# Performance work log

Hardware: AMD Instinct MI355X
Metric: run time of the kernel (lower is better)

## Reference

```python
import jax, jax.numpy as jnp
import numpy as np

N, E, F = 50000, 1_600_000, 128
EPS = 1e-5
DATASET_NUM = 1.0


def _glorot(k, shape):
    lim = jnp.sqrt(6.0 / (shape[0] + shape[1]))
    return jax.random.uniform(k, shape, jnp.float32, -lim, lim)


def setup_inputs() -> dict:
    key = jax.random.key(0)
    ks = jax.random.split(key, 24)
    inp = {
        "x": jax.random.normal(ks[0], (N, F), jnp.float32),
        "noise": jax.random.normal(ks[1], (N, F), jnp.float32),
        "edge_index": jax.random.randint(ks[2], (2, E), 0, N, jnp.int64),
        # ChebConv K=2 weights: W0 (T_0 = x term), W1 (T_1 = L_hat x term)
        "W1_0": _glorot(ks[3], (F, 64)),  "W1_1": _glorot(ks[4], (F, 64)),  "b1": jnp.zeros((64,), jnp.float32),
        "g1": jnp.ones((64,), jnp.float32), "be1": jnp.zeros((64,), jnp.float32),
        "W2_0": _glorot(ks[5], (64, 16)), "W2_1": _glorot(ks[6], (64, 16)), "b2": jnp.zeros((16,), jnp.float32),
        "W3_0": _glorot(ks[7], (16, 64)), "W3_1": _glorot(ks[8], (16, 64)), "b3": jnp.zeros((64,), jnp.float32),
        "g3": jnp.ones((64,), jnp.float32), "be3": jnp.zeros((64,), jnp.float32),
        "W4_0": _glorot(ks[9], (64, F)),  "W4_1": _glorot(ks[10], (64, F)), "b4": jnp.zeros((F,), jnp.float32),
    }
    return inp


def reference(x, noise, edge_index, W1_0, W1_1, b1, g1, be1,
              W2_0, W2_1, b2, W3_0, W3_1, b3, g3, be3, W4_0, W4_1, b4):
    src, dst = edge_index[0], edge_index[1]
    n = x.shape[0]

    # train-mode noise injection: x + dataset_num * randn * x.mean()
    x = x + DATASET_NUM * noise * jnp.mean(x)

    # symmetric normalization; with lambda_max=2 the scaled Laplacian is -A_norm
    deg = jax.ops.segment_sum(jnp.ones_like(src, dtype=x.dtype), dst, num_segments=n)
    dinv = jnp.where(deg > 0, jax.lax.rsqrt(jnp.maximum(deg, 1.0)), 0.0)
    w_e = dinv[src] * dinv[dst]  # [E]

    def cheb(h, W0, W1, b):
        # T_0 = h ; T_1 = L_hat h = -A_norm h  (K=2 ChebConv)
        tx1 = -jax.ops.segment_sum(w_e[:, None] * h[src], dst, num_segments=n)
        return h @ W0 + tx1 @ W1 + b

    def bn(h, g, be):
        mu = jnp.mean(h, axis=0)
        var = jnp.mean((h - mu) ** 2, axis=0)
        return g * (h - mu) * jax.lax.rsqrt(var + EPS) + be

    h1 = jax.nn.relu(bn(cheb(x, W1_0, W1_1, b1), g1, be1))
    h2 = cheb(h1, W2_0, W2_1, b2)
    h3 = jax.nn.relu(bn(cheb(h2, W3_0, W3_1, b3), g3, be3))
    return cheb(h3, W4_0, W4_1, b4)
```

## Files before the change

kernel.cpp:

```cpp
#include <hip/hip_runtime.h>

#define NNODES 50000
#define NEDGES 1600000
#define FEAT   128
#define EPSV   1e-5f
#define NBUCK  ((NNODES + 511) / 512)

typedef _Float16 h8 __attribute__((ext_vector_type(8)));
typedef _Float16 h4 __attribute__((ext_vector_type(4)));

__device__ __forceinline__ float4 f4fma(float s, float4 w, float4 a) {
  a.x = fmaf(s, w.x, a.x); a.y = fmaf(s, w.y, a.y);
  a.z = fmaf(s, w.z, a.z); a.w = fmaf(s, w.w, a.w);
  return a;
}

__global__ __launch_bounds__(256) void sum_kernel(const float* __restrict__ x,
                                                  float* __restrict__ out, int n4) {
  const float4* x4 = (const float4*)x;
  float s = 0.f;
  for (int i = blockIdx.x * blockDim.x + threadIdx.x; i < n4; i += gridDim.x * blockDim.x) {
    float4 v = x4[i];
    s += v.x + v.y + v.z + v.w;
  }
  for (int off = 32; off > 0; off >>= 1) s += __shfl_down(s, off);
  __shared__ float ls[4];
  int wid = threadIdx.x >> 6;
  if ((threadIdx.x & 63) == 0) ls[wid] = s;
  __syncthreads();
  if (threadIdx.x == 0) atomicAdd(out, ls[0] + ls[1] + ls[2] + ls[3]);
}

__global__ __launch_bounds__(256) void degree_kernel(const int* __restrict__ ei,
                                                     int* __restrict__ degi, int ne) {
  int e = blockIdx.x * blockDim.x + threadIdx.x;
  if (e < ne) atomicAdd(&degi[ei[NEDGES + e]], 1);
}

__global__ __launch_bounds__(256) void dinv_kernel(const int* __restrict__ degi,
                                                   float* __restrict__ dinv, int n) {
  int i = blockIdx.x * blockDim.x + threadIdx.x;
  if (i < n) dinv[i] = (degi[i] > 0) ? rsqrtf((float)degi[i]) : 0.f;
}

__global__ __launch_bounds__(1024) void scan1_kernel(const int* __restrict__ cnt,
                                                     int* __restrict__ exc,
                                                     int* __restrict__ bsum, int n) {
  __shared__ int s[1024];
  int tid = threadIdx.x;
  int i = blockIdx.x * 1024 + tid;
  int v = (i < n) ? cnt[i] : 0;
  int val = v;
  s[tid] = v;
  __syncthreads();
  for (int off = 1; off < 1024; off <<= 1) {
    int t = (tid >= off) ? s[tid - off] : 0;
    __syncthreads();
    val += t;
    s[tid] = val;
    __syncthreads();
  }
  if (i < n) exc[i] = val - v;
  if (tid == 1023) bsum[blockIdx.x] = val;
}

__global__ __launch_bounds__(256) void scan2_kernel(int* __restrict__ bsum, int nb) {
  __shared__ int s[256];
  int tid = threadIdx.x;
  int v = (tid < nb) ? bsum[tid] : 0;
  int val = v;
  s[tid] = v;
  __syncthreads();
  for (int off = 1; off < 256; off <<= 1) {
    int t = (tid >= off) ? s[tid - off] : 0;
    __syncthreads();
    val += t;
    s[tid] = val;
    __syncthreads();
  }
  if (tid < nb) bsum[tid] = val - v;
}

__global__ __launch_bounds__(256) void scan3_kernel(int* __restrict__ row_ptr,
                                                    const int* __restrict__ bsum,
                                                    int* __restrict__ cursor,
                                                    int* __restrict__ gcur, int n) {
  int i = blockIdx.x * blockDim.x + threadIdx.x;
  if (i < n) {
    int v = row_ptr[i] + bsum[i >> 10];
    row_ptr[i] = v;
    cursor[i] = v;
    if ((i & 511) == 0) gcur[i >> 9] = v;
  } else if (i == n) {
    row_ptr[n] = NEDGES;
  }
}

__global__ __launch_bounds__(256) void binA_kernel(const int* __restrict__ ei,
                                                   int* __restrict__ gcur,
                                                   unsigned int* __restrict__ gstage,
                                                   int ne) {
  __shared__ int hist[NBUCK];
  __shared__ int prefix[NBUCK + 1];
  __shared__ int offs[NBUCK];
  __shared__ int gbase[NBUCK];
  __shared__ unsigned int stag[4096];
  const int tid = threadIdx.x;
  const int c0 = blockIdx.x * 4096;
  for (int b = tid; b < NBUCK; b += 256) hist[b] = 0;
  __syncthreads();
  for (int i = tid; i < 4096; i += 256) {
    int e = c0 + i;
    if (e < ne) atomicAdd(&hist[ei[NEDGES + e] >> 9], 1);
  }
  __syncthreads();
  if (tid == 0) {
    int s = 0;
    for (int b = 0; b < NBUCK; ++b) { prefix[b] = s; s += hist[b]; }
    prefix[NBUCK] = s;
  }
  __syncthreads();
  if (tid < NBUCK) {
    offs[tid] = prefix[tid];
    gbase[tid] = atomicAdd(&gcur[tid], hist[tid]);
  }
  __syncthreads();
  for (int i = tid; i < 4096; i += 256) {
    int e = c0 + i;
    if (e < ne) {
      int s = ei[e];
      int d = ei[NEDGES + e];
      int b = d >> 9;
      int p = atomicAdd(&offs[b], 1);
      stag[p] = (unsigned int)s | ((unsigned int)(d & 511) << 16);
    }
  }
  __syncthreads();
  const int total = prefix[NBUCK];
  for (int j = tid; j < total; j += 256) {
    int lo = 0, hi = NBUCK;
    while (hi - lo > 1) {
      int mid = (lo + hi) >> 1;
      if (prefix[mid] <= j) lo = mid; else hi = mid;
    }
    gstage[gbase[lo] + (j - prefix[lo])] = stag[j];
  }
}

__global__ __launch_bounds__(1024) void binB_kernel(const unsigned int* __restrict__ gstage,
                                                    const int* __restrict__ row_ptr,
                                                    const float* __restrict__ dinv,
                                                    int* __restrict__ cursor,
                                                    int2* __restrict__ ep, int n) {
  const int b = blockIdx.x;
  const int node0 = b << 9;
  const int node1 = min(n, node0 + 512);
  const int start = row_ptr[node0];
  const int end = row_ptr[node1];
  for (int i = start + threadIdx.x; i < end; i += 1024) {
    unsigned int v = gstage[i];
    int s = (int)(v & 0xFFFFu);
    int d = node0 + (int)(v >> 16);
    float w = dinv[s] * dinv[d];
    int pos = atomicAdd(&cursor[d], 1);
    ep[pos] = make_int2(s, __float_as_int(w));
  }
}

template <int F, bool ADD, bool STATS, bool BNIN, bool OUTH>
__global__ __launch_bounds__(256) void spmm_kernel(
    const int* __restrict__ row_ptr, const int2* __restrict__ ep,
    const _Float16* __restrict__ gsrc, const float* __restrict__ addL,
    const float* __restrict__ bias,
    const float* __restrict__ stats_in, const float* __restrict__ gin,
    const float* __restrict__ bein, float* __restrict__ stats_out,
    void* __restrict__ outv, int n) {
  constexpr int LPE = F / 8;
  constexpr int EPC = 64 / LPE;
  constexpr int LG  = (LPE == 2) ? 1 : 3;
  __shared__ float sst[STATS ? 2 * F : 1];
  const int tid = threadIdx.x;
  if (STATS) {
    if (tid < 2 * F) sst[tid] = 0.f;
    __syncthreads();
  }
  const int lane = tid & 63;
  const int wv = tid >> 6;
  const int sub = lane & (LPE - 1);
  const int g = lane >> LG;
  const int f0 = sub * 8;
  float scl[8], sht[8];
  if (BNIN) {
    const float inv_n = 1.0f / (float)n;
#pragma unroll
    for (int j = 0; j < 8; ++j) {
      int f = f0 + j;
      float mu = stats_in[f] * inv_n;
      float var = stats_in[F + f] * inv_n - mu * mu;
      float s = gin[f] * rsqrtf(var + EPSV);
      scl[j] = s;
      sht[j] = bein[f] - mu * s;
    }
  }
  for (int node = blockIdx.x * 4 + wv; node < n; node += gridDim.x * 4) {
    float acc[8] = {};
    const int beg = row_ptr[node], end = row_ptr[node + 1];
    int e = beg + g;
    while (e < end) {
      int2 s0 = ep[e];
      bool p1 = (e + EPC) < end;
      int2 s1 = ep[p1 ? e + EPC : e];
      float w0 = __int_as_float(s0.y);
      float w1 = p1 ? __int_as_float(s1.y) : 0.f;
      h8 r0 = *(const h8*)(gsrc + (size_t)s0.x * F + f0);
      h8 r1 = *(const h8*)(gsrc + (size_t)s1.x * F + f0);
#pragma unroll
      for (int j = 0; j < 8; ++j) {
        float v0 = (float)r0[j], v1 = (float)r1[j];
        if (BNIN) {
          v0 = fmaxf(fmaf(v0, scl[j], sht[j]), 0.f);
          v1 = fmaxf(fmaf(v1, scl[j], sht[j]), 0.f);
        }
        acc[j] = fmaf(w0, v0, acc[j]);
        acc[j] = fmaf(w1, v1, acc[j]);
      }
      e += 2 * EPC;
    }
#pragma unroll
    for (int m = LPE; m < 64; m <<= 1) {
#pragma unroll
      for (int j = 0; j < 8; ++j) acc[j] += __shfl_xor(acc[j], m);
    }
    if (lane < LPE) {
      float o[8];
      if (ADD) {
        float4 a0 = *(const float4*)&addL[(size_t)node * F + f0];
        float4 a1 = *(const float4*)&addL[(size_t)node * F + f0 + 4];
        float4 b0 = *(const float4*)&bias[f0];
        float4 b1 = *(const float4*)&bias[f0 + 4];
        o[0] = a0.x + b0.x - acc[0]; o[1] = a0.y + b0.y - acc[1];
        o[2] = a0.z + b0.z - acc[2]; o[3] = a0.w + b0.w - acc[3];
        o[4] = a1.x + b1.x - acc[4]; o[5] = a1.y + b1.y - acc[5];
        o[6] = a1.z + b1.z - acc[6]; o[7] = a1.w + b1.w - acc[7];
      } else {
#pragma unroll
        for (int j = 0; j < 8; ++j) o[j] = -acc[j];
      }
      if (OUTH) {
        h8 ho;
#pragma unroll
        for (int j = 0; j < 8; ++j) ho[j] = (_Float16)o[j];
        *(h8*)((_Float16*)outv + (size_t)node * F + f0) = ho;
      } else {
        float* op = (float*)outv + (size_t)node * F + f0;
        *(float4*)op = make_float4(o[0], o[1], o[2], o[3]);
        *(float4*)(op + 4) = make_float4(o[4], o[5], o[6], o[7]);
      }
      if (STATS) {
#pragma unroll
        for (int j = 0; j < 8; ++j) {
          atomicAdd(&sst[f0 + j], o[j]);
          atomicAdd(&sst[F + f0 + j], o[j] * o[j]);
        }
      }
    }
  }
  if (STATS) {
    __syncthreads();
    if (tid < 2 * F) atomicAdd(&stats_out[tid], sst[tid]);
  }
}

template <int K, int NB, bool ROWCAT, bool BIAS, bool BNIN, bool STATS, bool NOISE,
          bool A1H, int OMODE>
__global__ __launch_bounds__(256) void gemm_kernel(
    const void* __restrict__ A1, const float* __restrict__ A2,
    const float* __restrict__ W0, const float* __restrict__ W1,
    const float* __restrict__ bias, int col0, int wnt, int ostride, int ocol0,
    const float* __restrict__ noise, const float* __restrict__ sumv,
    const float* __restrict__ stats_in, const float* __restrict__ gin,
    const float* __restrict__ bein, float* __restrict__ stats_out,
    void* __restrict__ outv, void* __restrict__ out2, int n) {
  constexpr int TC  = NB / 4;
  constexpr int RG  = 256 / TC;
  constexpr int RPT = 4;
  constexpr int RPB = RG * RPT;
  constexpr int AP  = K + 4;
  constexpr int KB  = ROWCAT ? K / 2 : K;
  __shared__ float wl[K * NB];
  __shared__ float al[RPB * AP];
  __shared__ float sarr[BNIN ? KB : 1];
  __shared__ float tarr[BNIN ? KB : 1];
  __shared__ float sst[STATS ? 2 * NB : 1];
  const int tid = threadIdx.x;
  if (STATS && tid < 2 * NB) sst[tid] = 0.f;
  if (BNIN) {
    const float inv_n = 1.0f / (float)n;
    for (int f = tid; f < KB; f += 256) {
      float mu = stats_in[f] * inv_n;
      float var = stats_in[KB + f] * inv_n - mu * mu;
      float s = gin[f] * rsqrtf(var + EPSV);
      sarr[f] = s;
      tarr[f] = bein[f] - mu * s;
    }
  }
  float mean = 0.f;
  if (NOISE) mean = sumv[0] * (1.0f / (float)(NNODES * FEAT));

  for (int i = tid; i < K * NB; i += 256) {
    int k = i / NB, j = i - k * NB;
    int jg = col0 + j;
    float v;
    if (ROWCAT) v = (k < K / 2) ? W0[k * wnt + jg] : W1[(k - K / 2) * wnt + jg];
    else        v = (jg < wnt / 2) ? W0[k * (wnt / 2) + jg] : W1[k * (wnt / 2) + (jg - wnt / 2)];
    wl[i] = v;
  }
  __syncthreads();

  const int row0 = blockIdx.x * RPB;
  for (int i = tid; i < RPB * K; i += 256) {
    int r = i / K, k = i - r * K;
    int gr = row0 + r;
    float v = 0.f;
    if (gr < n) {
      if (ROWCAT) {
        if (k < K / 2) {
          v = A1H ? (float)((const _Float16*)A1)[(size_t)gr * (K / 2) + k]
                  : ((const float*)A1)[(size_t)gr * (K / 2) + k];
          if (BNIN) v = fmaxf(fmaf(v, sarr[k], tarr[k]), 0.f);
        } else {
          v = A2[(size_t)gr * (K / 2) + (k - K / 2)];
        }
      } else {
        v = A1H ? (float)((const _Float16*)A1)[(size_t)gr * K + k]
                : ((const float*)A1)[(size_t)gr * K + k];
        if (BNIN) v = fmaxf(fmaf(v, sarr[k], tarr[k]), 0.f);
        if (NOISE) v = fmaf(noise[(size_t)gr * K + k], mean, v);
      }
    }
    al[r * AP + k] = v;
  }
  __syncthreads();

  const int jt = (tid % TC) * 4;
  const int rbase = (tid / TC) * RPT;
  float4 acc[RPT];
#pragma unroll
  for (int rr = 0; rr < RPT; ++rr) acc[rr] = make_float4(0.f, 0.f, 0.f, 0.f);
  const float4* wl4 = (const float4*)wl;
  const int jt4 = jt >> 2;
#pragma unroll 4
  for (int k0 = 0; k0 < K; k0 += 4) {
    float4 w0 = wl4[(k0 + 0) * TC + jt4];
    float4 w1 = wl4[(k0 + 1) * TC + jt4];
    float4 w2 = wl4[(k0 + 2) * TC + jt4];
    float4 w3 = wl4[(k0 + 3) * TC + jt4];
#pragma unroll
    for (int rr = 0; rr < RPT; ++rr) {
      float4 a = *(const float4*)&al[(rbase + rr) * AP + k0];
      acc[rr] = f4fma(a.x, w0, acc[rr]);
      acc[rr] = f4fma(a.y, w1, acc[rr]);
      acc[rr] = f4fma(a.z, w2, acc[rr]);
      acc[rr] = f4fma(a.w, w3, acc[rr]);
    }
  }
  float4 b4 = make_float4(0.f, 0.f, 0.f, 0.f);
  if (BIAS) b4 = *(const float4*)&bias[col0 + jt];
  float sl[4] = {}, ql[4] = {};
#pragma unroll
  for (int rr = 0; rr < RPT; ++rr) {
    int gr = row0 + rbase + rr;
    if (gr < n) {
      float4 o;
      o.x = acc[rr].x + b4.x; o.y = acc[rr].y + b4.y;
      o.z = acc[rr].z + b4.z; o.w = acc[rr].w + b4.w;
      if (OMODE == 0) {
        *(float4*)((float*)outv + (size_t)gr * ostride + ocol0 + jt) = o;
      } else if (OMODE == 1) {
        h4 ho; ho[0] = (_Float16)o.x; ho[1] = (_Float16)o.y;
        ho[2] = (_Float16)o.z; ho[3] = (_Float16)o.w;
        *(h4*)((_Float16*)outv + (size_t)gr * ostride + ocol0 + jt) = ho;
      } else {
        if (jt < 16) {
          *(float4*)((float*)outv + (size_t)gr * 16 + jt) = o;
        } else {
          h4 ho; ho[0] = (_Float16)o.x; ho[1] = (_Float16)o.y;
          ho[2] = (_Float16)o.z; ho[3] = (_Float16)o.w;
          *(h4*)((_Float16*)out2 + (size_t)gr * 16 + (jt - 16)) = ho;
        }
      }
      if (STATS) {
        sl[0] += o.x; ql[0] += o.x * o.x; sl[1] += o.y; ql[1] += o.y * o.y;
        sl[2] += o.z; ql[2] += o.z * o.z; sl[3] += o.w; ql[3] += o.w * o.w;
      }
    }
  }
  if (STATS) {
#pragma unroll
    for (int j = 0; j < 4; ++j) {
      atomicAdd(&sst[jt + j], sl[j]);
      atomicAdd(&sst[NB + jt + j], ql[j]);
    }
    __syncthreads();
    if (tid < 2 * NB) atomicAdd(&stats_out[tid], sst[tid]);
  }
}

extern "C" void kernel_launch(void* const* d_in, const int* in_sizes, int n_in,
                              void* d_out, int out_size, void* d_ws, size_t ws_size,
                              hipStream_t stream) {
  const float* x     = (const float*)d_in[0];
  const float* noise = (const float*)d_in[1];
  const int*   ei    = (const int*)d_in[2];
  const float* W1_0 = (const float*)d_in[3];
  const float* W1_1 = (const float*)d_in[4];
  const float* b1   = (const float*)d_in[5];
  const float* g1   = (const float*)d_in[6];
  const float* be1  = (const float*)d_in[7];
  const float* W2_0 = (const float*)d_in[8];
  const float* W2_1 = (const float*)d_in[9];
  const float* b2   = (const float*)d_in[10];
  const float* W3_0 = (const float*)d_in[11];
  const float* W3_1 = (const float*)d_in[12];
  const float* b3   = (const float*)d_in[13];
  const float* g3   = (const float*)d_in[14];
  const float* be3  = (const float*)d_in[15];
  const float* W4_0 = (const float*)d_in[16];
  const float* W4_1 = (const float*)d_in[17];
  const float* b4   = (const float*)d_in[18];
  float* out = (float*)d_out;

  char* p = (char*)d_ws;
  size_t off = 0;
  auto alloc = [&](size_t b) -> void* {
    void* r = p + off;
    off += (b + 255) & ~(size_t)255;
    return r;
  };
  float* s_sum  = (float*)alloc(4);
  float* stats0 = (float*)alloc(2 * 64 * 4);
  float* stats1 = (float*)alloc(2 * 64 * 4);
  int*   degi   = (int*)alloc(sizeof(int) * NNODES);
  size_t zero_bytes = off;
  float*     dinv    = (float*)alloc(sizeof(float) * NNODES);
  int*       row_ptr = (int*)alloc(sizeof(int) * (NNODES + 1));
  int*       bsum    = (int*)alloc(256 * sizeof(int));
  int*       cursor  = (int*)alloc(sizeof(int) * NNODES);
  int*       gcur    = (int*)alloc(sizeof(int) * NBUCK);
  int2*      ep      = (int2*)alloc(8ULL * NEDGES);
  float*     zzL     = (float*)alloc(4ULL * NNODES * 64);
  _Float16*  zzRh    = (_Float16*)alloc(2ULL * NNODES * 64);
  float*     h1      = (float*)alloc(4ULL * NNODES * 64);
  _Float16*  zz2Rh   = (_Float16*)alloc(2ULL * NNODES * 16);
  _Float16*  h2      = (_Float16*)alloc(2ULL * NNODES * 16);
  _Float16*  h3h     = (_Float16*)alloc(2ULL * NNODES * 64);
  float*     agg4    = zzL;

  unsigned int* gstage = (unsigned int*)out;
  float* zz2L = out;
  float* agg3 = out + (size_t)NNODES * 16;

  hipMemsetAsync(d_ws, 0, zero_bytes, stream);

  int n4 = NNODES * FEAT / 4;
  sum_kernel<<<2048, 256, 0, stream>>>(x, s_sum, n4);
  degree_kernel<<<(NEDGES + 255) / 256, 256, 0, stream>>>(ei, degi, NEDGES);
  dinv_kernel<<<(NNODES + 255) / 256, 256, 0, stream>>>(degi, dinv, NNODES);
  scan1_kernel<<<(NNODES + 1023) / 1024, 1024, 0, stream>>>(degi, row_ptr, bsum, NNODES);
  scan2_kernel<<<1, 256, 0, stream>>>(bsum, (NNODES + 1023) / 1024);
  scan3_kernel<<<(NNODES + 256) / 256, 256, 0, stream>>>(row_ptr, bsum, cursor, gcur, NNODES);
  binA_kernel<<<(NEDGES + 4095) / 4096, 256, 0, stream>>>(ei, gcur, gstage, NEDGES);
  binB_kernel<<<NBUCK, 1024, 0, stream>>>(gstage, row_ptr, dinv, cursor, ep, NNODES);

  gemm_kernel<128, 64, false, false, false, false, true, false, 0>
      <<<(NNODES + 63) / 64, 256, 0, stream>>>(
      x, nullptr, W1_0, W1_1, nullptr, 0, 128, 64, 0,
      noise, s_sum, nullptr, nullptr, nullptr, nullptr, zzL, nullptr, NNODES);
  gemm_kernel<128, 64, false, false, false, false, true, false, 1>
      <<<(NNODES + 63) / 64, 256, 0, stream>>>(
      x, nullptr, W1_0, W1_1, nullptr, 64, 128, 64, 0,
      noise, s_sum, nullptr, nullptr, nullptr, nullptr, zzRh, nullptr, NNODES);
  spmm_kernel<64, true, true, false, false><<<2048, 256, 0, stream>>>(
      row_ptr, ep, zzRh, zzL, b1, nullptr, nullptr, nullptr, stats0, h1, NNODES);

  gemm_kernel<64, 32, false, false, true, false, false, false, 2>
      <<<(NNODES + 127) / 128, 256, 0, stream>>>(
      h1, nullptr, W2_0, W2_1, nullptr, 0, 32, 16, 0,
      nullptr, nullptr, stats0, g1, be1, nullptr, zz2L, zz2Rh, NNODES);
  spmm_kernel<16, true, false, false, true><<<2048, 256, 0, stream>>>(
      row_ptr, ep, zz2Rh, zz2L, b2, nullptr, nullptr, nullptr, nullptr, h2, NNODES);

  spmm_kernel<16, false, false, false, false><<<2048, 256, 0, stream>>>(
      row_ptr, ep, h2, nullptr, nullptr, nullptr, nullptr, nullptr, nullptr, agg3, NNODES);
  gemm_kernel<32, 64, true, true, false, true, false, true, 1>
      <<<(NNODES + 63) / 64, 256, 0, stream>>>(
      h2, agg3, W3_0, W3_1, b3, 0, 64, 64, 0,
      nullptr, nullptr, nullptr, nullptr, nullptr, stats1, h3h, nullptr, NNODES);

  spmm_kernel<64, false, false, true, false><<<2048, 256, 0, stream>>>(
      row_ptr, ep, h3h, nullptr, nullptr, stats1, g3, be3, nullptr, agg4, NNODES);
  gemm_kernel<128, 64, true, true, true, false, false, true, 0>
      <<<(NNODES + 63) / 64, 256, 0, stream>>>(
      h3h, agg4, W4_0, W4_1, b4, 0, 128, 128, 0,
      nullptr, nullptr, stats1, g3, be3, nullptr, out, nullptr, NNODES);
  gemm_kernel<128, 64, true, true, true, false, false, true, 0>
      <<<(NNODES + 63) / 64, 256, 0, stream>>>(
      h3h, agg4, W4_0, W4_1, b4, 64, 128, 128, 64,
      nullptr, nullptr, stats1, g3, be3, nullptr, out, nullptr, NNODES);
}
```

Baseline: 688.5 us.

## Factor edge weights into source/destination scaling and compress edge list to 16-bit

Drops the per-edge normalisation weight by factoring dinv[src]*dinv[dst] into a pre-scale of source rows (in the GEMM epilogue or a dual-output SpMM) and a post-scale by dinv[dst]. The edge list shrinks from 8-byte (index, weight) pairs to 16-bit source indices, and several intermediates (zzL, h1, agg3, agg4) move from fp32 to fp16. This cuts gather and streaming bandwidth in the SpMMs and GEMMs, at the cost of more fp16 rounding and reliance on node indices fitting in 16 bits. The BN-input SpMM still gathers dinv per edge, because the ReLU prevents pre-scaling there.

```diff
diff --git a/kernel.cpp b/kernel.cpp
--- a/kernel.cpp
+++ b/kernel.cpp
@@ -149,9 +149,8 @@
 
 __global__ __launch_bounds__(1024) void binB_kernel(const unsigned int* __restrict__ gstage,
                                                     const int* __restrict__ row_ptr,
-                                                    const float* __restrict__ dinv,
                                                     int* __restrict__ cursor,
-                                                    int2* __restrict__ ep, int n) {
+                                                    unsigned short* __restrict__ ep, int n) {
   const int b = blockIdx.x;
   const int node0 = b << 9;
   const int node1 = min(n, node0 + 512);
@@ -161,20 +160,19 @@
     unsigned int v = gstage[i];
     int s = (int)(v & 0xFFFFu);
     int d = node0 + (int)(v >> 16);
-    float w = dinv[s] * dinv[d];
     int pos = atomicAdd(&cursor[d], 1);
-    ep[pos] = make_int2(s, __float_as_int(w));
-  }
-}
-
-template <int F, bool ADD, bool STATS, bool BNIN, bool OUTH>
+    ep[pos] = (unsigned short)s;
+  }
+}
+
+template <int F, bool ADD, bool ADDH, bool STATS, bool BNIN, bool GDINV, bool DUAL>
 __global__ __launch_bounds__(256) void spmm_kernel(
-    const int* __restrict__ row_ptr, const int2* __restrict__ ep,
-    const _Float16* __restrict__ gsrc, const float* __restrict__ addL,
-    const float* __restrict__ bias,
+    const int* __restrict__ row_ptr, const unsigned short* __restrict__ ep,
+    const _Float16* __restrict__ gsrc, const void* __restrict__ addL,
+    const float* __restrict__ bias, const float* __restrict__ dinv,
     const float* __restrict__ stats_in, const float* __restrict__ gin,
     const float* __restrict__ bein, float* __restrict__ stats_out,
-    void* __restrict__ outv, int n) {
+    _Float16* __restrict__ outv, _Float16* __restrict__ out2, int n) {
   constexpr int LPE = F / 8;
   constexpr int EPC = 64 / LPE;
   constexpr int LG  = (LPE == 2) ? 1 : 3;
@@ -207,13 +205,16 @@
     const int beg = row_ptr[node], end = row_ptr[node + 1];
     int e = beg + g;
     while (e < end) {
-      int2 s0 = ep[e];
+      int s0 = ep[e];
       bool p1 = (e + EPC) < end;
-      int2 s1 = ep[p1 ? e + EPC : e];
-      float w0 = __int_as_float(s0.y);
-      float w1 = p1 ? __int_as_float(s1.y) : 0.f;
-      h8 r0 = *(const h8*)(gsrc + (size_t)s0.x * F + f0);
-      h8 r1 = *(const h8*)(gsrc + (size_t)s1.x * F + f0);
+      int s1 = ep[p1 ? e + EPC : e];
+      float dv0 = 0.f, dv1 = 0.f;
+      if (GDINV) {
+        dv0 = dinv[s0];
+        dv1 = p1 ? dinv[s1] : 0.f;
+      }
+      h8 r0 = *(const h8*)(gsrc + (size_t)s0 * F + f0);
+      h8 r1 = *(const h8*)(gsrc + (size_t)s1 * F + f0);
 #pragma unroll
       for (int j = 0; j < 8; ++j) {
         float v0 = (float)r0[j], v1 = (float)r1[j];
@@ -221,8 +222,13 @@
           v0 = fmaxf(fmaf(v0, scl[j], sht[j]), 0.f);
           v1 = fmaxf(fmaf(v1, scl[j], sht[j]), 0.f);
         }
-        acc[j] = fmaf(w0, v0, acc[j]);
-        acc[j] = fmaf(w1, v1, acc[j]);
+        if (GDINV) {
+          acc[j] = fmaf(dv0, v0, acc[j]);
+          acc[j] = fmaf(dv1, v1, acc[j]);
+        } else {
+          acc[j] += v0;
+          acc[j] += p1 ? v1 : 0.f;
+        }
       }
       e += 2 * EPC;
     }
@@ -232,29 +238,27 @@
       for (int j = 0; j < 8; ++j) acc[j] += __shfl_xor(acc[j], m);
     }
     if (lane < LPE) {
+      const float dn = dinv[node];
       float o[8];
-      if (ADD) {
-        float4 a0 = *(const float4*)&addL[(size_t)node * F + f0];
-        float4 a1 = *(const float4*)&addL[(size_t)node * F + f0 + 4];
-        float4 b0 = *(const float4*)&bias[f0];
-        float4 b1 = *(const float4*)&bias[f0 + 4];
-        o[0] = a0.x + b0.x - acc[0]; o[1] = a0.y + b0.y - acc[1];
-        o[2] = a0.z + b0.z - acc[2]; o[3] = a0.w + b0.w - acc[3];
-        o[4] = a1.x + b1.x - acc[4]; o[5] = a1.y + b1.y - acc[5];
-        o[6] = a1.z + b1.z - acc[6]; o[7] = a1.w + b1.w - acc[7];
-      } else {
-#pragma unroll
-        for (int j = 0; j < 8; ++j) o[j] = -acc[j];
-      }
-      if (OUTH) {
-        h8 ho;
-#pragma unroll
-        for (int j = 0; j < 8; ++j) ho[j] = (_Float16)o[j];
-        *(h8*)((_Float16*)outv + (size_t)node * F + f0) = ho;
-      } else {
-        float* op = (float*)outv + (size_t)node * F + f0;
-        *(float4*)op = make_float4(o[0], o[1], o[2], o[3]);
-        *(float4*)(op + 4) = make_float4(o[4], o[5], o[6], o[7]);
+#pragma unroll
+      for (int j = 0; j < 8; ++j) {
+        float base = 0.f;
+        if (ADD) {
+          float a = ADDH ? (float)((const _Float16*)addL)[(size_t)node * F + f0 + j]
+                         : ((const float*)addL)[(size_t)node * F + f0 + j];
+          base = a + bias[f0 + j];
+        }
+        o[j] = base - dn * acc[j];
+      }
+      h8 ho;
+#pragma unroll
+      for (int j = 0; j < 8; ++j) ho[j] = (_Float16)o[j];
+      *(h8*)(outv + (size_t)node * F + f0) = ho;
+      if (DUAL) {
+        h8 hs;
+#pragma unroll
+        for (int j = 0; j < 8; ++j) hs[j] = (_Float16)(dn * o[j]);
+        *(h8*)(out2 + (size_t)node * F + f0) = hs;
       }
       if (STATS) {
 #pragma unroll
@@ -272,14 +276,15 @@
 }
 
 template <int K, int NB, bool ROWCAT, bool BIAS, bool BNIN, bool STATS, bool NOISE,
-          bool A1H, int OMODE>
+          bool A1H, bool A2H, bool RSCL, int OMODE>
 __global__ __launch_bounds__(256) void gemm_kernel(
-    const void* __restrict__ A1, const float* __restrict__ A2,
+    const void* __restrict__ A1, const void* __restrict__ A2,
     const float* __restrict__ W0, const float* __restrict__ W1,
     const float* __restrict__ bias, int col0, int wnt, int ostride, int ocol0,
     const float* __restrict__ noise, const float* __restrict__ sumv,
     const float* __restrict__ stats_in, const float* __restrict__ gin,
     const float* __restrict__ bein, float* __restrict__ stats_out,
+    const float* __restrict__ rowscl,
     void* __restrict__ outv, void* __restrict__ out2, int n) {
   constexpr int TC  = NB / 4;
   constexpr int RG  = 256 / TC;
@@ -329,7 +334,8 @@
                   : ((const float*)A1)[(size_t)gr * (K / 2) + k];
           if (BNIN) v = fmaxf(fmaf(v, sarr[k], tarr[k]), 0.f);
         } else {
-          v = A2[(size_t)gr * (K / 2) + (k - K / 2)];
+          v = A2H ? (float)((const _Float16*)A2)[(size_t)gr * (K / 2) + (k - K / 2)]
+                  : ((const float*)A2)[(size_t)gr * (K / 2) + (k - K / 2)];
         }
       } else {
         v = A1H ? (float)((const _Float16*)A1)[(size_t)gr * K + k]
@@ -374,18 +380,19 @@
       float4 o;
       o.x = acc[rr].x + b4.x; o.y = acc[rr].y + b4.y;
       o.z = acc[rr].z + b4.z; o.w = acc[rr].w + b4.w;
+      float fac = RSCL ? rowscl[gr] : 1.f;
       if (OMODE == 0) {
         *(float4*)((float*)outv + (size_t)gr * ostride + ocol0 + jt) = o;
       } else if (OMODE == 1) {
-        h4 ho; ho[0] = (_Float16)o.x; ho[1] = (_Float16)o.y;
-        ho[2] = (_Float16)o.z; ho[3] = (_Float16)o.w;
+        h4 ho; ho[0] = (_Float16)(o.x * fac); ho[1] = (_Float16)(o.y * fac);
+        ho[2] = (_Float16)(o.z * fac); ho[3] = (_Float16)(o.w * fac);
         *(h4*)((_Float16*)outv + (size_t)gr * ostride + ocol0 + jt) = ho;
       } else {
         if (jt < 16) {
           *(float4*)((float*)outv + (size_t)gr * 16 + jt) = o;
         } else {
-          h4 ho; ho[0] = (_Float16)o.x; ho[1] = (_Float16)o.y;
-          ho[2] = (_Float16)o.z; ho[3] = (_Float16)o.w;
+          h4 ho; ho[0] = (_Float16)(o.x * fac); ho[1] = (_Float16)(o.y * fac);
+          ho[2] = (_Float16)(o.z * fac); ho[3] = (_Float16)(o.w * fac);
           *(h4*)((_Float16*)out2 + (size_t)gr * 16 + (jt - 16)) = ho;
         }
       }
@@ -442,23 +449,24 @@
   float* stats1 = (float*)alloc(2 * 64 * 4);
   int*   degi   = (int*)alloc(sizeof(int) * NNODES);
   size_t zero_bytes = off;
-  float*     dinv    = (float*)alloc(sizeof(float) * NNODES);
-  int*       row_ptr = (int*)alloc(sizeof(int) * (NNODES + 1));
-  int*       bsum    = (int*)alloc(256 * sizeof(int));
-  int*       cursor  = (int*)alloc(sizeof(int) * NNODES);
-  int*       gcur    = (int*)alloc(sizeof(int) * NBUCK);
-  int2*      ep      = (int2*)alloc(8ULL * NEDGES);
-  float*     zzL     = (float*)alloc(4ULL * NNODES * 64);
-  _Float16*  zzRh    = (_Float16*)alloc(2ULL * NNODES * 64);
-  float*     h1      = (float*)alloc(4ULL * NNODES * 64);
-  _Float16*  zz2Rh   = (_Float16*)alloc(2ULL * NNODES * 16);
-  _Float16*  h2      = (_Float16*)alloc(2ULL * NNODES * 16);
-  _Float16*  h3h     = (_Float16*)alloc(2ULL * NNODES * 64);
-  float*     agg4    = zzL;
+  float*          dinv    = (float*)alloc(sizeof(float) * NNODES);
+  int*            row_ptr = (int*)alloc(sizeof(int) * (NNODES + 1));
+  int*            bsum    = (int*)alloc(256 * sizeof(int));
+  int*            cursor  = (int*)alloc(sizeof(int) * NNODES);
+  int*            gcur    = (int*)alloc(sizeof(int) * NBUCK);
+  unsigned short* ep16    = (unsigned short*)alloc(2ULL * NEDGES);
+  _Float16*       zzLh    = (_Float16*)alloc(2ULL * NNODES * 64);
+  _Float16*       zzRh    = (_Float16*)alloc(2ULL * NNODES * 64);
+  _Float16*       h1h     = (_Float16*)alloc(2ULL * NNODES * 64);
+  _Float16*       zz2Rh   = (_Float16*)alloc(2ULL * NNODES * 16);
+  _Float16*       h2h     = (_Float16*)alloc(2ULL * NNODES * 16);
+  _Float16*       h2sh    = (_Float16*)alloc(2ULL * NNODES * 16);
+  _Float16*       h3h     = (_Float16*)alloc(2ULL * NNODES * 64);
+  _Float16*       agg4h   = zzLh;
 
   unsigned int* gstage = (unsigned int*)out;
-  float* zz2L = out;
-  float* agg3 = out + (size_t)NNODES * 16;
+  float*    zz2L  = out;
+  _Float16* agg3h = (_Float16*)(out + (size_t)NNODES * 16);
 
   hipMemsetAsync(d_ws, 0, zero_bytes, stream);
 
@@ -470,41 +478,45 @@
   scan2_kernel<<<1, 256, 0, stream>>>(bsum, (NNODES + 1023) / 1024);
   scan3_kernel<<<(NNODES + 256) / 256, 256, 0, stream>>>(row_ptr, bsum, cursor, gcur, NNODES);
   binA_kernel<<<(NEDGES + 4095) / 4096, 256, 0, stream>>>(ei, gcur, gstage, NEDGES);
-  binB_kernel<<<NBUCK, 1024, 0, stream>>>(gstage, row_ptr, dinv, cursor, ep, NNODES);
-
-  gemm_kernel<128, 64, false, false, false, false, true, false, 0>
+  binB_kernel<<<NBUCK, 1024, 0, stream>>>(gstage, row_ptr, cursor, ep16, NNODES);
+
+  gemm_kernel<128, 64, false, false, false, false, true, false, false, false, 1>
       <<<(NNODES + 63) / 64, 256, 0, stream>>>(
       x, nullptr, W1_0, W1_1, nullptr, 0, 128, 64, 0,
-      noise, s_sum, nullptr, nullptr, nullptr, nullptr, zzL, nullptr, NNODES);
-  gemm_kernel<128, 64, false, false, false, false, true, false, 1>
+      noise, s_sum, nullptr, nullptr, nullptr, nullptr, nullptr, zzLh, nullptr, NNODES);
+  gemm_kernel<128, 64, false, false, false, false, true, false, false, true, 1>
       <<<(NNODES + 63) / 64, 256, 0, stream>>>(
       x, nullptr, W1_0, W1_1, nullptr, 64, 128, 64, 0,
-      noise, s_sum, nullptr, nullptr, nullptr, nullptr, zzRh, nullptr, NNODES);
-  spmm_kernel<64, true, true, false, false><<<2048, 256, 0, stream>>>(
-      row_ptr, ep, zzRh, zzL, b1, nullptr, nullptr, nullptr, stats0, h1, NNODES);
-
-  gemm_kernel<64, 32, false, false, true, false, false, false, 2>
+      noise, s_sum, nullptr, nullptr, nullptr, nullptr, dinv, zzRh, nullptr, NNODES);
+  spmm_kernel<64, true, true, true, false, false, false><<<2048, 256, 0, stream>>>(
+      row_ptr, ep16, zzRh, zzLh, b1, dinv, nullptr, nullptr, nullptr, stats0,
+      h1h, nullptr, NNODES);
+
+  gemm_kernel<64, 32, false, false, true, false, false, true, false, true, 2>
       <<<(NNODES + 127) / 128, 256, 0, stream>>>(
-      h1, nullptr, W2_0, W2_1, nullptr, 0, 32, 16, 0,
-      nullptr, nullptr, stats0, g1, be1, nullptr, zz2L, zz2Rh, NNODES);
-  spmm_kernel<16, true, false, false, true><<<2048, 256, 0, stream>>>(
-      row_ptr, ep, zz2Rh, zz2L, b2, nullptr, nullptr, nullptr, nullptr, h2, NNODES);
-
-  spmm_kernel<16, false, false, false, false><<<2048, 256, 0, stream>>>(
-      row_ptr, ep, h2, nullptr, nullptr, nullptr, nullptr, nullptr, nullptr, agg3, NNODES);
-  gemm_kernel<32, 64, true, true, false, true, false, true, 1>
+      h1h, nullptr, W2_0, W2_1, nullptr, 0, 32, 16, 0,
+      nullptr, nullptr, stats0, g1, be1, nullptr, dinv, zz2L, zz2Rh, NNODES);
+  spmm_kernel<16, true, false, false, false, false, true><<<2048, 256, 0, stream>>>(
+      row_ptr, ep16, zz2Rh, zz2L, b2, dinv, nullptr, nullptr, nullptr, nullptr,
+      h2h, h2sh, NNODES);
+
+  spmm_kernel<16, false, false, false, false, false, false><<<2048, 256, 0, stream>>>(
+      row_ptr, ep16, h2sh, nullptr, nullptr, dinv, nullptr, nullptr, nullptr, nullptr,
+      agg3h, nullptr, NNODES);
+  gemm_kernel<32, 64, true, true, false, true, false, true, true, false, 1>
       <<<(NNODES + 63) / 64, 256, 0, stream>>>(
-      h2, agg3, W3_0, W3_1, b3, 0, 64, 64, 0,
-      nullptr, nullptr, nullptr, nullptr, nullptr, stats1, h3h, nullptr, NNODES);
-
-  spmm_kernel<64, false, false, true, false><<<2048, 256, 0, stream>>>(
-      row_ptr, ep, h3h, nullptr, nullptr, stats1, g3, be3, nullptr, agg4, NNODES);
-  gemm_kernel<128, 64, true, true, true, false, false, true, 0>
+      h2h, agg3h, W3_0, W3_1, b3, 0, 64, 64, 0,
+      nullptr, nullptr, nullptr, nullptr, nullptr, stats1, nullptr, h3h, nullptr, NNODES);
+
+  spmm_kernel<64, false, false, false, true, true, false><<<2048, 256, 0, stream>>>(
+      row_ptr, ep16, h3h, nullptr, nullptr, dinv, stats1, g3, be3, nullptr,
+      agg4h, nullptr, NNODES);
+  gemm_kernel<128, 64, true, true, true, false, false, true, true, false, 0>
       <<<(NNODES + 63) / 64, 256, 0, stream>>>(
-      h3h, agg4, W4_0, W4_1, b4, 0, 128, 128, 0,
-      nullptr, nullptr, stats1, g3, be3, nullptr, out, nullptr, NNODES);
-  gemm_kernel<128, 64, true, true, true, false, false, true, 0>
+      h3h, agg4h, W4_0, W4_1, b4, 0, 128, 128, 0,
+      nullptr, nullptr, stats1, g3, be3, nullptr, nullptr, out, nullptr, NNODES);
+  gemm_kernel<128, 64, true, true, true, false, false, true, true, false, 0>
       <<<(NNODES + 63) / 64, 256, 0, stream>>>(
-      h3h, agg4, W4_0, W4_1, b4, 64, 128, 128, 64,
-      nullptr, nullptr, stats1, g3, be3, nullptr, out, nullptr, NNODES);
-}
+      h3h, agg4h, W4_0, W4_1, b4, 64, 128, 128, 64,
+      nullptr, nullptr, stats1, g3, be3, nullptr, nullptr, out, nullptr, NNODES);
+}
```

Measured after the change: 685.4 us. No clear change (-0.4%).
